# Kernel tuning notes

Measured on AMD Instinct MI355X. Metric: run time of the kernel, lower is better.

The kernel has to match this reference:

```python
import jax, jax.numpy as jnp
import numpy as np
from jax import lax

ANCHOR_AREAS = (128.0**2, 256.0**2, 512.0**2)
ASPECT_RATIOS = (0.5, 1.0, 2.0)
STRIDE = 32.0                      # resnet backbone: get_orig_stat maps fm -> input via x*32
PRE_NMS_TOP_N = 2000
POST_NMS_TOP_N = 100
NMS_IOU_T = 0.7
SCORE_T = 0.1
MIN_SCALE = 0.01
BBOX_XFORM_CLIP = float(np.log(1000.0 / 16.0))


def make_anchors(H, W):
    # anchors laid out in (H, W, A) order to match the offset permutation below
    sizes = []
    for area in ANCHOR_AREAS:
        for r in ASPECT_RATIOS:          # aspect_ratio = w / h
            sizes.append((np.sqrt(area * r), np.sqrt(area / r)))
    sizes = jnp.asarray(np.asarray(sizes, dtype=np.float32))  # [A, 2] (w, h)
    cy = (jnp.arange(H, dtype=jnp.float32) + 0.5) * STRIDE
    cx = (jnp.arange(W, dtype=jnp.float32) + 0.5) * STRIDE
    cyg, cxg = jnp.meshgrid(cy, cx, indexing='ij')             # [H, W]
    cxg = cxg[:, :, None]
    cyg = cyg[:, :, None]
    w = sizes[:, 0]
    h = sizes[:, 1]
    anchors = jnp.stack([cxg - w / 2, cyg - h / 2, cxg + w / 2, cyg + h / 2], axis=-1)
    return anchors.reshape(-1, 4)                              # [H*W*A, 4] xyxy


def decode_boxes(anchors, offsets):
    # anchors [N,4], offsets [B,N,4] (tx, ty, tw, th) -> boxes [B,N,4] xyxy
    wa = anchors[:, 2] - anchors[:, 0]
    ha = anchors[:, 3] - anchors[:, 1]
    cxa = anchors[:, 0] + 0.5 * wa
    cya = anchors[:, 1] + 0.5 * ha
    tx, ty = offsets[..., 0], offsets[..., 1]
    tw = jnp.minimum(offsets[..., 2], BBOX_XFORM_CLIP)
    th = jnp.minimum(offsets[..., 3], BBOX_XFORM_CLIP)
    px = tx * wa + cxa
    py = ty * ha + cya
    pw = jnp.exp(tw) * wa
    ph = jnp.exp(th) * ha
    return jnp.stack([px - pw / 2, py - ph / 2, px + pw / 2, py + ph / 2], axis=-1)


def box_iou(a, b):
    area_a = (a[:, 2] - a[:, 0]) * (a[:, 3] - a[:, 1])
    area_b = (b[:, 2] - b[:, 0]) * (b[:, 3] - b[:, 1])
    lt = jnp.maximum(a[:, None, :2], b[None, :, :2])
    rb = jnp.minimum(a[:, None, 2:], b[None, :, 2:])
    wh = jnp.clip(rb - lt, 0.0)
    inter = wh[..., 0] * wh[..., 1]
    return inter / (area_a[:, None] + area_b[None, :] - inter + 1e-9)


def nms_single(boxes, scores):
    # boxes [P,4] sorted by descending score; invalid entries carry score -1
    P = boxes.shape[0]
    iou = box_iou(boxes, boxes)
    idx = jnp.arange(P)

    def body(i, keep):
        sup = (iou[i] > NMS_IOU_T) & (idx > i)
        return jnp.where(keep[i], keep & (~sup), keep)

    keep = lax.stop_gradient(lax.fori_loop(0, P, body, scores > 0.0))
    kept_scores = jnp.where(keep, scores, -1.0)
    top_s, top_i = lax.top_k(kept_scores, POST_NMS_TOP_N)
    return boxes[top_i], top_s


def rpn_forward(features, W1, b1, W2, b2, W3, b3):
    B, Cin, H, W = features.shape
    A = W3.shape[0]
    # 3x3 sliding conv + ReLU
    t = lax.conv_general_dilated(
        features, W1, window_strides=(1, 1), padding='SAME',
        dimension_numbers=('NCHW', 'OIHW', 'NCHW'))
    t = jax.nn.relu(t + b1[None, :, None, None])
    # 1x1 sibling heads as channel contractions
    offs = jnp.einsum('bchw,oc->bohw', t, W2) + b2[None, :, None, None]   # [B, A*4, H, W]
    logits = jnp.einsum('bchw,oc->bohw', t, W3) + b3[None, :, None, None]  # [B, A, H, W]
    # reorder to per-anchor layout (H, W, A)
    offs = offs.reshape(B, A, 4, H, W).transpose(0, 3, 4, 1, 2).reshape(B, -1, 4)
    scores = jax.nn.sigmoid(logits.transpose(0, 2, 3, 1).reshape(B, -1))  # [B, N]
    anchors = make_anchors(H, W)
    boxes = decode_boxes(anchors, offs)                                    # [B, N, 4]
    # clip to image boundary (handle_cross_boundary_boxes during testing)
    img_w, img_h = W * STRIDE, H * STRIDE
    boxes = jnp.stack([
        jnp.clip(boxes[..., 0], 0.0, img_w),
        jnp.clip(boxes[..., 1], 0.0, img_h),
        jnp.clip(boxes[..., 2], 0.0, img_w),
        jnp.clip(boxes[..., 3], 0.0, img_h)], axis=-1)
    # score-threshold + min-scale filtering
    bw = boxes[..., 2] - boxes[..., 0]
    bh = boxes[..., 3] - boxes[..., 1]
    valid = (scores >= SCORE_T) & (bw > MIN_SCALE * img_w) & (bh > MIN_SCALE * img_h)
    masked = jnp.where(valid, scores, -1.0)
    # pre-NMS top-k, then per-image NMS + post-NMS top-n
    top_s, top_i = lax.top_k(masked, PRE_NMS_TOP_N)                        # [B, P]
    top_boxes = jnp.take_along_axis(boxes, top_i[..., None], axis=1)       # [B, P, 4]
    out_boxes, out_scores = jax.vmap(nms_single)(top_boxes, top_s)
    return out_boxes, out_scores                                           # [B,100,4], [B,100]


def setup_inputs() -> dict:
    key = jax.random.key(0)
    ks = jax.random.split(key, 4)
    B, Cin, H, W = 8, 1024, 50, 50
    A = 9
    C = 512
    return {
        'features': jax.random.normal(ks[0], (B, Cin, H, W), jnp.float32),
        'W1': jax.random.normal(ks[1], (C, Cin, 3, 3), jnp.float32) * 0.01,
        'b1': jnp.zeros((C,), jnp.float32),
        'W2': jax.random.normal(ks[2], (A * 4, C), jnp.float32) * 0.01,
        'b2': jnp.zeros((A * 4,), jnp.float32),
        'W3': jax.random.normal(ks[3], (A, C), jnp.float32) * 0.01,
        'b3': jnp.zeros((A,), jnp.float32),
    }


def reference(features, W1, b1, W2, b2, W3, b3):
    return rpn_forward(features, W1, b1, W2, b2, W3, b3)
```

## Files before the change

kernel.cpp:

```cpp
#include <hip/hip_runtime.h>
#include <cstdint>

#define NB 8
#define CIN 1024
#define HDIM 50
#define WDIM 50
#define COUT 512
#define NA 9
#define NANCH (HDIM*WDIM*NA)
#define PRE_N 2000
#define POST_N 100

typedef __attribute__((ext_vector_type(8))) short bf16x8;
typedef __attribute__((ext_vector_type(4))) float f32x4;
typedef __attribute__((ext_vector_type(16))) float f32x16;
typedef __attribute__((ext_vector_type(8))) unsigned short ushort8v;

constexpr size_t TPLANE    = 20578304;
constexpr size_t OFF_TPH   = 0;
constexpr size_t OFF_TPL   = 20578304;
constexpr size_t OFF_BOXES = 41156608;
constexpr size_t OFF_KEYS  = 44036608;
constexpr size_t OFF_TBOX  = 45476608;
constexpr size_t OFF_TS    = 45732608;
constexpr size_t OFF_SUP   = 45796608;
constexpr size_t QDIM      = 2976;
constexpr size_t PLSTRIDE  = QDIM * 8;
constexpr size_t PPLANE    = 48758784;
constexpr size_t OFF_PH    = 49892864;
constexpr size_t OFF_PL    = OFF_PH + PPLANE;
constexpr size_t WPLANE    = 9437184;
constexpr size_t OFF_WH    = 147410432;
constexpr size_t OFF_WL    = OFF_WH + WPLANE;

__device__ __forceinline__ void split2bf16(float v, unsigned short &hi, unsigned short &lo) {
    unsigned int u = __float_as_uint(v);
    unsigned int r = u + 0x7FFFu + ((u >> 16) & 1u);
    hi = (unsigned short)(r >> 16);
    float hf = __uint_as_float(((unsigned int)hi) << 16);
    float lf = v - hf;
    unsigned int u2 = __float_as_uint(lf);
    unsigned int r2 = u2 + 0x7FFFu + ((u2 >> 16) & 1u);
    lo = (unsigned short)(r2 >> 16);
}

__device__ __forceinline__ void gl_lds(const unsigned short* g, unsigned short* l) {
    __builtin_amdgcn_global_load_lds(
        (const __attribute__((address_space(1))) unsigned int*)(const void*)g,
        (__attribute__((address_space(3))) unsigned int*)(void*)l,
        16, 0, 0);
}

__global__ __launch_bounds__(256) void prep_all(const float* __restrict__ f,
                                                const float* __restrict__ W1,
                                                unsigned short* __restrict__ Ph,
                                                unsigned short* __restrict__ Pl,
                                                unsigned short* __restrict__ Wh,
                                                unsigned short* __restrict__ Wl) {
    int blk = blockIdx.x;
    if (blk < 5952) {
        int id = blk * 256 + threadIdx.x;
        int q = id % (int)QDIM; int r = id / (int)QDIM;
        int cic = r % 64; int b = r / 64;
        int pp = q - 53;
        int rr = pp / 52, cc = pp - rr * 52;
        int h = rr - 1, w = cc - 1;
        bool inb = (pp >= 0) && (pp < 2704) && (h >= 0) && (h < HDIM) && (w >= 0) && (w < WDIM);
        ushort8v hv0, lv0, hv1, lv1;
#pragma unroll
        for (int j = 0; j < 16; ++j) {
            float v = 0.f;
            if (inb) v = f[(((size_t)b * CIN + cic * 16 + j) * HDIM + h) * WDIM + w];
            unsigned short hi, lo;
            split2bf16(v, hi, lo);
            if (j < 8) { hv0[j] = hi; lv0[j] = lo; }
            else       { hv1[j - 8] = hi; lv1[j - 8] = lo; }
        }
        size_t b0 = ((size_t)((b * 64 + cic) * 2 + 0)) * PLSTRIDE + (size_t)q * 8;
        size_t b1 = ((size_t)((b * 64 + cic) * 2 + 1)) * PLSTRIDE + (size_t)q * 8;
        *(ushort8v*)&Ph[b0] = hv0;
        *(ushort8v*)&Ph[b1] = hv1;
        *(ushort8v*)&Pl[b0] = lv0;
        *(ushort8v*)&Pl[b1] = lv1;
    } else {
        int id = (blk - 5952) * 256 + threadIdx.x;
        int co = id % 64; int r = id / 64;
        int cic = r % 64; int cot = r / 64;
        int cog = cot * 64 + co;
        const float* src = W1 + ((size_t)cog * CIN + cic * 16) * 9;
        float v[144];
#pragma unroll
        for (int i = 0; i < 36; ++i) {
            float4 x = ((const float4*)src)[i];
            v[i * 4 + 0] = x.x; v[i * 4 + 1] = x.y; v[i * 4 + 2] = x.z; v[i * 4 + 3] = x.w;
        }
#pragma unroll
        for (int tap = 0; tap < 9; ++tap) {
            ushort8v hv0, lv0, hv1, lv1;
#pragma unroll
            for (int j = 0; j < 16; ++j) {
                unsigned short hi, lo;
                split2bf16(v[j * 9 + tap], hi, lo);
                if (j < 8) { hv0[j] = hi; lv0[j] = lo; }
                else       { hv1[j - 8] = hi; lv1[j - 8] = lo; }
            }
            size_t base = (((size_t)(cot * 64 + cic) * 9 + tap) * 2) * 512;
            *(ushort8v*)&Wh[base + co * 8]       = hv0;
            *(ushort8v*)&Wh[base + 512 + co * 8] = hv1;
            *(ushort8v*)&Wl[base + co * 8]       = lv0;
            *(ushort8v*)&Wl[base + 512 + co * 8] = lv1;
        }
    }
}


#define MFMA12(A_, B_)                                                               \
    do {                                                                             \
        _Pragma("unroll") for (int s_ = 0; s_ < 3; ++s_)                             \
        _Pragma("unroll") for (int jm_ = 0; jm_ < 2; ++jm_)                          \
        _Pragma("unroll") for (int jn_ = 0; jn_ < 2; ++jn_) {                        \
            const bf16x8 &av_ = (s_ == 2) ? A_[jm_][1] : A_[jm_][0];                 \
            const bf16x8 &bv_ = (s_ == 1) ? B_[jn_][1] : B_[jn_][0];                 \
            acc[jm_][jn_] = __builtin_amdgcn_mfma_f32_32x32x16_bf16(                 \
                av_, bv_, acc[jm_][jn_], 0, 0, 0);                                   \
        }                                                                            \
    } while (0)

#define LOADF(A_, B_, TL_)                                                           \
    do {                                                                             \
        const int dlt_ = (tg - 1) * 52 + ((TL_) - 1);                                \
        _Pragma("unroll") for (int jm_ = 0; jm_ < 2; ++jm_) {                        \
            int ad_ = ((wv * 2 + jm_) * 32 + lm + dlt_ + 53) * 8;                    \
            A_[jm_][0] = *(const bf16x8*)&bA[(0 * 2 + lk) * 3072 + ad_];             \
            A_[jm_][1] = *(const bf16x8*)&bA[(1 * 2 + lk) * 3072 + ad_];             \
        }                                                                            \
        _Pragma("unroll") for (int jn_ = 0; jn_ < 2; ++jn_) {                        \
            int bd_ = (TL_) * 1024 + lk * 512 + (jn_ * 32 + lm) * 8;                 \
            B_[jn_][0] = *(const bf16x8*)&bB[bd_];                                   \
            B_[jn_][1] = *(const bf16x8*)&bB[3072 + bd_];                            \
        }                                                                            \
    } while (0)

__global__ __launch_bounds__(256, 2) void conv_mfma(const unsigned short* __restrict__ FPh,
                                                    const unsigned short* __restrict__ FPl,
                                                    const unsigned short* __restrict__ WPh,
                                                    const unsigned short* __restrict__ WPl,
                                                    const float* __restrict__ b1,
                                                    unsigned short* __restrict__ Tph,
                                                    unsigned short* __restrict__ Tpl) {
    extern __shared__ unsigned short smem[];
    unsigned short* const Abase = smem;
    unsigned short* const Bbase = smem + 24576;

    int blk = blockIdx.x;
    int logical = (blk & 7) * 88 + (blk >> 3);
    int cot = logical & 7;
    int ptile = (logical >> 3) % 11;
    int b = logical / 88;
    int co0 = cot * 64;
    int P0 = 32 + ptile * 256;

    int t = threadIdx.x, wv = t >> 6, ln = t & 63;
    int lm = ln & 31, lk = ln >> 5;

    f32x16 acc[2][2];
#pragma unroll
    for (int jm = 0; jm < 2; ++jm)
#pragma unroll
        for (int jn = 0; jn < 2; ++jn)
#pragma unroll
            for (int rg = 0; rg < 16; ++rg) acc[jm][jn][rg] = 0.f;

    auto stageA = [&](int buf, int cic, int ac) {
        int hl = ac / 12, lkc = (ac / 6) & 1, s = ac % 6;
        const unsigned short* pl = hl ? FPl : FPh;
        const unsigned short* src = pl
            + ((size_t)((b * 64 + cic) * 2 + lkc)) * PLSTRIDE
            + (size_t)P0 * 8 + s * 512 + ln * 8;
        gl_lds(src, &Abase[buf * 12288 + (hl * 2 + lkc) * 3072 + s * 512]);
    };
    auto stageB = [&](int buf, int cic, int tg, int c) {
        int hl = c / 6, j = c % 6;
        const unsigned short* pl = hl ? WPl : WPh;
        const unsigned short* src = pl + (size_t)(cot * 64 + cic) * 9216
            + (size_t)(tg * 6 + j) * 512 + ln * 8;
        gl_lds(src, &Bbase[buf * 6144 + hl * 3072 + j * 512]);
    };

#pragma unroll
    for (int k = 0; k < 9; ++k) {
        int id = wv * 9 + k;
        if (id < 24) stageA(0, 0, id);
        else         stageB(0, 0, 0, id - 24);
    }
    __syncthreads();

#pragma unroll 1
    for (int cic = 0; cic < 64; ++cic) {
        int abuf = cic & 1;
        bool haveA = (cic + 1 < 64);
#pragma unroll
        for (int tg = 0; tg < 3; ++tg) {
            int bbuf = (cic + tg) & 1;
            int cicb = (tg == 2) ? cic + 1 : cic;
            int tgn  = (tg == 2) ? 0 : tg + 1;
            bool haveB = (cicb < 64);
#pragma unroll
            for (int k = 0; k < 5; ++k) {
                int id = wv * 5 + k;
                if (id < 12) { if (haveB) stageB(bbuf ^ 1, cicb, tgn, id); }
                else         { if (haveA) stageA(abuf ^ 1, cic + 1, tg * 8 + (id - 12)); }
            }
            const unsigned short* bA = Abase + abuf * 12288;
            const unsigned short* bB = Bbase + bbuf * 6144;

            bf16x8 aX[2][2], bX[2][2], aY[2][2], bY[2][2];
            LOADF(aX, bX, 0);
            __builtin_amdgcn_s_setprio(1);
            LOADF(aY, bY, 1);
            MFMA12(aX, bX);
            LOADF(aX, bX, 2);
            MFMA12(aY, bY);
            MFMA12(aX, bX);
            __builtin_amdgcn_s_setprio(0);

            __builtin_amdgcn_sched_group_barrier(0x070, 5, 0);
            __builtin_amdgcn_sched_group_barrier(0x100, 8, 0);
#pragma unroll
            for (int g = 0; g < 8; ++g) {
                __builtin_amdgcn_sched_group_barrier(0x008, 3, 0);
                __builtin_amdgcn_sched_group_barrier(0x100, 2, 0);
            }
            __builtin_amdgcn_sched_group_barrier(0x008, 12, 0);

            __syncthreads();
        }
    }

#pragma unroll
    for (int jn = 0; jn < 2; ++jn) {
        int co = co0 + jn * 32 + lm;
        float bv = b1[co];
#pragma unroll
        for (int jm = 0; jm < 2; ++jm) {
#pragma unroll
            for (int rg = 0; rg < 16; ++rg) {
                int mrow = (rg & 3) + 8 * (rg >> 2) + 4 * lk;
                int pp = P0 + (wv * 2 + jm) * 32 + mrow;
                int rr = pp / 52, cc = pp - rr * 52;
                int h = rr - 1, w = cc - 1;
                if ((unsigned)h < HDIM && (unsigned)w < WDIM) {
                    float v = fmaxf(acc[jm][jn][rg] + bv, 0.f);
                    unsigned short hi, lo;
                    split2bf16(v, hi, lo);
                    int px = b * 2500 + h * 50 + w;
                    size_t sa = (((((size_t)(px >> 7) * 16 + (co >> 5)) * 8 + ((px >> 4) & 7)) * 4
                                  + ((co >> 3) & 3)) * 16 + (px & 15)) * 8 + (co & 7);
                    Tph[sa] = hi;
                    Tpl[sa] = lo;
                }
            }
        }
    }
}

__global__ __launch_bounds__(256) void proj_decode_mfma(const unsigned short* __restrict__ Tph,
                                                        const unsigned short* __restrict__ Tpl,
                                                        const float* __restrict__ W2,
                                                        const float* __restrict__ b2,
                                                        const float* __restrict__ W3,
                                                        const float* __restrict__ b3,
                                                        float* __restrict__ boxes,
                                                        unsigned long long* __restrict__ keys) {
    __shared__ unsigned short sTh[4096], sTl[4096];
    __shared__ unsigned short sWh[1536], sWl[1536];
    __shared__ float pout[128 * 46];

    int blk = blockIdx.x;
    int px0 = blk * 128;
    int t = threadIdx.x, wv = t >> 6, ln = t & 63;
    int lm = ln & 15, q = ln >> 4;

    f32x4 acc[2][3];
#pragma unroll
    for (int jm = 0; jm < 2; ++jm)
#pragma unroll
        for (int nf = 0; nf < 3; ++nf) acc[jm][nf] = (f32x4){0.f, 0.f, 0.f, 0.f};

#pragma unroll 1
    for (int cc16 = 0; cc16 < 16; ++cc16) {
        __syncthreads();
        size_t base = ((size_t)blk * 16 + cc16) * 4096;
        if (wv == 0) {
#pragma unroll
            for (int s = 0; s < 4; ++s) gl_lds(Tph + base + s * 512 + ln * 8, &sTh[s * 512]);
        } else if (wv == 1) {
#pragma unroll
            for (int s = 4; s < 8; ++s) gl_lds(Tph + base + s * 512 + ln * 8, &sTh[s * 512]);
        } else if (wv == 2) {
#pragma unroll
            for (int s = 0; s < 4; ++s) gl_lds(Tpl + base + s * 512 + ln * 8, &sTl[s * 512]);
        } else {
#pragma unroll
            for (int s = 4; s < 8; ++s) gl_lds(Tpl + base + s * 512 + ln * 8, &sTl[s * 512]);
        }
        int c0 = cc16 * 32;
        for (int idx = t; idx < 1536; idx += 256) {
            int o = idx >> 5, ci = idx & 31;
            float v = 0.f;
            if (o < 36) v = W2[o * 512 + c0 + ci];
            else if (o < 45) v = W3[(o - 36) * 512 + c0 + ci];
            unsigned short hi, lo;
            split2bf16(v, hi, lo);
            int ad = (((o >> 4) * 4 + (ci >> 3)) * 16 + (o & 15)) * 8 + (ci & 7);
            sWh[ad] = hi; sWl[ad] = lo;
        }
        __syncthreads();

        bf16x8 a[2][2], bb[3][2];
#pragma unroll
        for (int jm = 0; jm < 2; ++jm) {
            int mf = wv * 2 + jm;
            int ad = ((mf * 4 + q) * 16 + lm) * 8;
            a[jm][0] = *(const bf16x8*)&sTh[ad];
            a[jm][1] = *(const bf16x8*)&sTl[ad];
        }
#pragma unroll
        for (int nf = 0; nf < 3; ++nf) {
            int ad = ((nf * 4 + q) * 16 + lm) * 8;
            bb[nf][0] = *(const bf16x8*)&sWh[ad];
            bb[nf][1] = *(const bf16x8*)&sWl[ad];
        }
#pragma unroll
        for (int jm = 0; jm < 2; ++jm)
#pragma unroll
            for (int nf = 0; nf < 3; ++nf) {
                acc[jm][nf] = __builtin_amdgcn_mfma_f32_16x16x32_bf16(a[jm][0], bb[nf][0], acc[jm][nf], 0, 0, 0);
                acc[jm][nf] = __builtin_amdgcn_mfma_f32_16x16x32_bf16(a[jm][0], bb[nf][1], acc[jm][nf], 0, 0, 0);
                acc[jm][nf] = __builtin_amdgcn_mfma_f32_16x16x32_bf16(a[jm][1], bb[nf][0], acc[jm][nf], 0, 0, 0);
            }
    }
    __syncthreads();
#pragma unroll
    for (int jm = 0; jm < 2; ++jm)
#pragma unroll
        for (int nf = 0; nf < 3; ++nf) {
            int o = nf * 16 + lm;
            if (o < 45) {
                float bias = (o < 36) ? b2[o] : b3[o - 36];
#pragma unroll
                for (int rg = 0; rg < 4; ++rg) {
                    int pxl = (wv * 2 + jm) * 16 + q * 4 + rg;
                    pout[pxl * 46 + o] = acc[jm][nf][rg] + bias;
                }
            }
        }
    __syncthreads();

    const float AW[9] = {90.50966799187809f, 128.0f, 181.01933598375618f,
                         181.01933598375618f, 256.0f, 362.03867196751236f,
                         362.03867196751236f, 512.0f, 724.0773439350247f};
    const float AH[9] = {181.01933598375618f, 128.0f, 90.50966799187809f,
                         362.03867196751236f, 256.0f, 181.01933598375618f,
                         724.0773439350247f, 512.0f, 362.03867196751236f};
    const float CLIPV = 4.135166556742356f;
    const float IMG = 1600.0f;

    for (int it = t; it < 128 * 9; it += 256) {
        int pxl = it / 9, a = it - pxl * 9;
        int pxg = px0 + pxl;
        if (pxg >= 20000) continue;
        int b = pxg / 2500, rem = pxg % 2500;
        int h = rem / 50, w = rem % 50;

        float tx = pout[pxl * 46 + a * 4 + 0];
        float ty = pout[pxl * 46 + a * 4 + 1];
        float tw = pout[pxl * 46 + a * 4 + 2];
        float th = pout[pxl * 46 + a * 4 + 3];
        float lg = pout[pxl * 46 + 36 + a];

        float s = 1.0f / (1.0f + expf(-lg));

        float cx = ((float)w + 0.5f) * 32.0f;
        float cy = ((float)h + 0.5f) * 32.0f;
        float x1a = cx - 0.5f * AW[a];
        float x2a = cx + 0.5f * AW[a];
        float y1a = cy - 0.5f * AH[a];
        float y2a = cy + 0.5f * AH[a];
        float waf = x2a - x1a;
        float haf = y2a - y1a;
        float cxa = x1a + 0.5f * waf;
        float cya = y1a + 0.5f * haf;

        float twc = tw < CLIPV ? tw : CLIPV;
        float thc = th < CLIPV ? th : CLIPV;
        float pxc = tx * waf + cxa;
        float pyc = ty * haf + cya;
        float pw  = expf(twc) * waf;
        float ph  = expf(thc) * haf;

        float x1 = pxc - 0.5f * pw;
        float y1 = pyc - 0.5f * ph;
        float x2 = pxc + 0.5f * pw;
        float y2 = pyc + 0.5f * ph;
        x1 = fminf(fmaxf(x1, 0.f), IMG);
        y1 = fminf(fmaxf(y1, 0.f), IMG);
        x2 = fminf(fmaxf(x2, 0.f), IMG);
        y2 = fminf(fmaxf(y2, 0.f), IMG);

        float bw = x2 - x1, bh = y2 - y1;
        bool valid = (s >= 0.1f) && (bw > 16.0f) && (bh > 16.0f);
        float m = valid ? s : -1.0f;

        int idx = (h * WDIM + w) * NA + a;
        size_t gi = (size_t)b * NANCH + idx;
        ((float4*)boxes)[gi] = make_float4(x1, y1, x2, y2);
        unsigned int u = __float_as_uint(m);
        unsigned int k32 = (u & 0x80000000u) ? ~u : (u | 0x80000000u);
        keys[gi] = ((unsigned long long)k32 << 15) | (unsigned long long)(32767 - idx);
    }
}

__global__ __launch_bounds__(1024) void select_sort_kernel(const unsigned long long* __restrict__ keys,
                                                           const float* __restrict__ boxes,
                                                           float* __restrict__ top_boxes,
                                                           float* __restrict__ top_s) {
    int b = blockIdx.x;
    int t = threadIdx.x;
    int wv = t >> 6;
    const unsigned long long* kb = keys + (size_t)b * NANCH;

    __shared__ unsigned int whist[16][256];
    __shared__ unsigned int hist[256];
    __shared__ int s_chosen, s_rnew;
    __shared__ unsigned int s_cnt;
    __shared__ unsigned long long skeys[2048];

    const int widths[6] = {8, 8, 8, 8, 8, 7};
    unsigned long long prefix = 0;
    int bitsdone = 0;
    int r = PRE_N;

    for (int p = 0; p < 6; ++p) {
        int width = widths[p];
        int bins = 1 << width;
        int shift = 47 - bitsdone - width;
        for (int i = t; i < 16 * 256; i += 1024) ((unsigned int*)whist)[i] = 0;
        __syncthreads();
        for (int i = t; i < NANCH; i += 1024) {
            unsigned long long k = kb[i];
            if ((k >> (47 - bitsdone)) == prefix)
                atomicAdd(&whist[wv][(unsigned)((k >> shift) & (unsigned long long)(bins - 1))], 1u);
        }
        __syncthreads();
        if (t < bins) {
            unsigned int s = 0;
#pragma unroll
            for (int w = 0; w < 16; ++w) s += whist[w][t];
            hist[t] = s;
        }
        __syncthreads();
        if (t == 0) {
            int acc = 0, chosen = 0, rnew = 1;
            for (int d = bins - 1; d >= 0; --d) {
                int hv = (int)hist[d];
                if (acc + hv >= r) { chosen = d; rnew = r - acc; break; }
                acc += hv;
            }
            s_chosen = chosen;
            s_rnew = rnew;
        }
        __syncthreads();
        prefix = (prefix << width) | (unsigned long long)s_chosen;
        bitsdone += width;
        r = s_rnew;
        __syncthreads();
    }
    unsigned long long Kst = prefix;

    if (t == 0) s_cnt = 0;
    __syncthreads();
    for (int i = t; i < NANCH; i += 1024) {
        unsigned long long k = kb[i];
        if (k >= Kst) {
            unsigned int p = atomicAdd(&s_cnt, 1u);
            if (p < 2048) skeys[p] = k;
        }
    }
    __syncthreads();
    unsigned int cnt = s_cnt;
    for (int i = t; i < 2048; i += 1024)
        if (i >= (int)cnt) skeys[i] = 0ull;
    for (int k = 2; k <= 2048; k <<= 1) {
        for (int j = k >> 1; j > 0; j >>= 1) {
            __syncthreads();
            for (int i = t; i < 2048; i += 1024) {
                int l = i ^ j;
                if (l > i) {
                    unsigned long long a = skeys[i], c = skeys[l];
                    bool up = ((i & k) == 0);
                    if (up ? (a < c) : (a > c)) { skeys[i] = c; skeys[l] = a; }
                }
            }
        }
    }
    __syncthreads();
    for (int i = t; i < PRE_N; i += 1024) {
        unsigned long long k = skeys[i];
        unsigned int k32 = (unsigned int)(k >> 15);
        float m = (k32 & 0x80000000u) ? __uint_as_float(k32 & 0x7FFFFFFFu)
                                      : __uint_as_float(~k32);
        unsigned int idx = 32767u - (unsigned int)(k & 32767ull);
        size_t gi = (size_t)b * NANCH + idx;
        top_s[b * PRE_N + i] = m;
        ((float4*)top_boxes)[b * PRE_N + i] = ((const float4*)boxes)[gi];
    }
}

__global__ __launch_bounds__(256) void sup_kernel(const float* __restrict__ top_boxes,
                                                  unsigned long long* __restrict__ supm) {
    int blk = blockIdx.x;
    int b = blk / 125;
    int chunk = blk % 125;
    int t = threadIdx.x;

    __shared__ float bx1[PRE_N], by1[PRE_N], bx2[PRE_N], by2[PRE_N];
    for (int i = t; i < PRE_N; i += 256) {
        float4 v = ((const float4*)top_boxes)[b * PRE_N + i];
        bx1[i] = v.x; by1[i] = v.y; bx2[i] = v.z; by2[i] = v.w;
    }
    __syncthreads();

    int wave = t >> 6, lane = t & 63;
    for (int rr = 0; rr < 4; ++rr) {
        int i = chunk * 16 + wave * 4 + rr;
        float ax1 = bx1[i], ay1 = by1[i], ax2 = bx2[i], ay2 = by2[i];
        float aarea = (ax2 - ax1) * (ay2 - ay1);
        for (int jw = 0; jw < 32; ++jw) {
            int j = jw * 64 + lane;
            bool sup = false;
            if (j > i && j < PRE_N) {
                float jx1 = bx1[j], jy1 = by1[j], jx2 = bx2[j], jy2 = by2[j];
                float ix1 = fmaxf(ax1, jx1), iy1 = fmaxf(ay1, jy1);
                float ix2 = fminf(ax2, jx2), iy2 = fminf(ay2, jy2);
                float iw = fmaxf(ix2 - ix1, 0.f);
                float ih = fmaxf(iy2 - iy1, 0.f);
                float inter = iw * ih;
                float barea = (jx2 - jx1) * (jy2 - jy1);
                float iou = inter / (aarea + barea - inter + 1e-9f);
                sup = iou > 0.7f;
            }
            unsigned long long m = __ballot(sup);
            if (lane == 0) supm[((size_t)b * PRE_N + i) * 32 + jw] = m;
        }
    }
}

__global__ __launch_bounds__(256) void nms_fin_kernel(const float* __restrict__ top_s,
                                                      const unsigned long long* __restrict__ supm,
                                                      const float* __restrict__ top_boxes,
                                                      float* __restrict__ out) {
    int b = blockIdx.x;
    int t = threadIdx.x;
    __shared__ unsigned int kw[64];
    __shared__ int wpre[65];

    if (t < 64) {
        int lane = t;
        unsigned int alive = 0;
        for (int q = 0; q < 32; ++q) {
            int i = lane * 32 + q;
            if (i < PRE_N && top_s[b * PRE_N + i] > 0.f) alive |= (1u << q);
        }
        const unsigned long long* sm = supm + (size_t)b * PRE_N * 32;
        const unsigned int* sup32 = (const unsigned int*)sm;

        for (int tt = 0; tt < 32; ++tt) {
            unsigned int alo = __shfl(alive, 2 * tt);
            unsigned int ahi = __shfl(alive, 2 * tt + 1);
            unsigned long long talive = (unsigned long long)alo | ((unsigned long long)ahi << 32);
            int i_row = tt * 64 + lane;
            unsigned long long rm = (i_row < PRE_N) ? sm[(size_t)i_row * 32 + tt] : 0ull;

            unsigned long long kept = 0, rem = talive;
            while (rem) {
                int j = __builtin_ctzll(rem);
                kept |= (1ull << j);
                unsigned long long rmj = __shfl(rm, j);
                rem &= ~rmj;
                rem &= ~(1ull << j);
            }

            unsigned int oracc = 0;
            unsigned long long kk = kept;
            while (kk) {
                int j0 = __builtin_ctzll(kk); kk &= kk - 1;
                int j1 = -1, j2 = -1, j3 = -1;
                if (kk) { j1 = __builtin_ctzll(kk); kk &= kk - 1; }
                if (kk) { j2 = __builtin_ctzll(kk); kk &= kk - 1; }
                if (kk) { j3 = __builtin_ctzll(kk); kk &= kk - 1; }
                unsigned int v0 = sup32[(size_t)(tt * 64 + j0) * 64 + lane];
                unsigned int v1 = (j1 >= 0) ? sup32[(size_t)(tt * 64 + j1) * 64 + lane] : 0u;
                unsigned int v2 = (j2 >= 0) ? sup32[(size_t)(tt * 64 + j2) * 64 + lane] : 0u;
                unsigned int v3 = (j3 >= 0) ? sup32[(size_t)(tt * 64 + j3) * 64 + lane] : 0u;
                oracc |= v0 | v1 | v2 | v3;
            }
            alive &= ~oracc;
            if (lane == 2 * tt)     alive = (unsigned int)kept;
            if (lane == 2 * tt + 1) alive = (unsigned int)(kept >> 32);
        }
        kw[lane] = alive;
    }
    __syncthreads();
    if (t == 0) {
        int run = 0;
        for (int w = 0; w < 64; ++w) { wpre[w] = run; run += __popc(kw[w]); }
        wpre[64] = run;
    }
    __syncthreads();
    int total = wpre[64];
    float* out_boxes  = out;
    float* out_scores = out + NB * POST_N * 4;
    for (int i = t; i < PRE_N; i += 256) {
        unsigned int w = kw[i >> 5];
        bool kept = (w >> (i & 31)) & 1u;
        int rk = wpre[i >> 5] + __popc(w & ((1u << (i & 31)) - 1u));
        int pos = kept ? rk : total + (i - rk);
        if (pos < POST_N) {
            out_scores[b * POST_N + pos] = kept ? top_s[b * PRE_N + i] : -1.0f;
            ((float4*)out_boxes)[b * POST_N + pos] = ((const float4*)top_boxes)[b * PRE_N + i];
        }
    }
}

extern "C" void kernel_launch(void* const* d_in, const int* in_sizes, int n_in,
                              void* d_out, int out_size, void* d_ws, size_t ws_size,
                              hipStream_t stream) {
    const float* features = (const float*)d_in[0];
    const float* W1 = (const float*)d_in[1];
    const float* b1 = (const float*)d_in[2];
    const float* W2 = (const float*)d_in[3];
    const float* b2 = (const float*)d_in[4];
    const float* W3 = (const float*)d_in[5];
    const float* b3 = (const float*)d_in[6];
    float* out = (float*)d_out;
    char* ws = (char*)d_ws;

    unsigned short* Tph = (unsigned short*)(ws + OFF_TPH);
    unsigned short* Tpl = (unsigned short*)(ws + OFF_TPL);
    float* boxes   = (float*)(ws + OFF_BOXES);
    unsigned long long* keys = (unsigned long long*)(ws + OFF_KEYS);
    float* top_boxes = (float*)(ws + OFF_TBOX);
    float* top_s     = (float*)(ws + OFF_TS);
    unsigned long long* supm = (unsigned long long*)(ws + OFF_SUP);
    unsigned short* FPh = (unsigned short*)(ws + OFF_PH);
    unsigned short* FPl = (unsigned short*)(ws + OFF_PL);
    unsigned short* WPh = (unsigned short*)(ws + OFF_WH);
    unsigned short* WPl = (unsigned short*)(ws + OFF_WL);

    static bool conv_attr_set = false;
    if (!conv_attr_set) {
        hipFuncSetAttribute(reinterpret_cast<const void*>(&conv_mfma),
                            hipFuncAttributeMaxDynamicSharedMemorySize, 73728);
        conv_attr_set = true;
    }

    prep_all<<<6080, 256, 0, stream>>>(features, W1, FPh, FPl, WPh, WPl);
    conv_mfma<<<704, 256, 73728, stream>>>(FPh, FPl, WPh, WPl, b1, Tph, Tpl);
    proj_decode_mfma<<<157, 256, 0, stream>>>(Tph, Tpl, W2, b2, W3, b3, boxes, keys);
    select_sort_kernel<<<NB, 1024, 0, stream>>>(keys, boxes, top_boxes, top_s);
    sup_kernel<<<NB * 125, 256, 0, stream>>>(top_boxes, supm);
    nms_fin_kernel<<<NB, 256, 0, stream>>>(top_s, supm, top_boxes, out);
}
```

Before: 1.083 ms.

## Rebalance conv staging, peel last K-step, early-exit radix select, widen NMS OR batch

The conv GEMM loop now gives every wave a fixed 3 B-tile and 2 A-tile stage (replacing the 5-per-wave split with idle slots) and peels the last input-channel chunk so it skips staging and scheduling barriers. The radix top-k select stops early once the candidate count at the current prefix fits in the 2048-entry sort buffer, saving histogram passes over all anchors. The NMS suppression OR loop batches 8 row loads instead of 4 for more memory-level parallelism. Early exit can admit more candidates into the bitonic sort, and the new staging split must still cover all tiles exactly.

New measurement: 1.001 ms. 1.08x faster.

```diff
diff --git a/kernel.cpp b/kernel.cpp
--- a/kernel.cpp
+++ b/kernel.cpp
@@ -51,6 +51,9 @@
         16, 0, 0);
 }
 
+struct StageOn  { static constexpr bool value = true;  };
+struct StageOff { static constexpr bool value = false; };
+
 __global__ __launch_bounds__(256) void prep_all(const float* __restrict__ f,
                                                 const float* __restrict__ W1,
                                                 unsigned short* __restrict__ Ph,
@@ -195,21 +198,21 @@
     }
     __syncthreads();
 
-#pragma unroll 1
-    for (int cic = 0; cic < 64; ++cic) {
+    auto do_cic = [&](int cic, auto stage_c) {
+        constexpr bool STAGE = decltype(stage_c)::value;
         int abuf = cic & 1;
-        bool haveA = (cic + 1 < 64);
 #pragma unroll
         for (int tg = 0; tg < 3; ++tg) {
             int bbuf = (cic + tg) & 1;
-            int cicb = (tg == 2) ? cic + 1 : cic;
-            int tgn  = (tg == 2) ? 0 : tg + 1;
-            bool haveB = (cicb < 64);
-#pragma unroll
-            for (int k = 0; k < 5; ++k) {
-                int id = wv * 5 + k;
-                if (id < 12) { if (haveB) stageB(bbuf ^ 1, cicb, tgn, id); }
-                else         { if (haveA) stageA(abuf ^ 1, cic + 1, tg * 8 + (id - 12)); }
+            if (STAGE || tg < 2) {
+                int cicb = (tg == 2) ? cic + 1 : cic;
+                int tgn  = (tg == 2) ? 0 : tg + 1;
+#pragma unroll
+                for (int j = 0; j < 3; ++j) stageB(bbuf ^ 1, cicb, tgn, wv * 3 + j);
+            }
+            if constexpr (STAGE) {
+#pragma unroll
+                for (int j = 0; j < 2; ++j) stageA(abuf ^ 1, cic + 1, tg * 8 + wv * 2 + j);
             }
             const unsigned short* bA = Abase + abuf * 12288;
             const unsigned short* bB = Bbase + bbuf * 6144;
@@ -224,18 +227,23 @@
             MFMA12(aX, bX);
             __builtin_amdgcn_s_setprio(0);
 
-            __builtin_amdgcn_sched_group_barrier(0x070, 5, 0);
-            __builtin_amdgcn_sched_group_barrier(0x100, 8, 0);
-#pragma unroll
-            for (int g = 0; g < 8; ++g) {
-                __builtin_amdgcn_sched_group_barrier(0x008, 3, 0);
-                __builtin_amdgcn_sched_group_barrier(0x100, 2, 0);
-            }
-            __builtin_amdgcn_sched_group_barrier(0x008, 12, 0);
-
+            if constexpr (STAGE) {
+                __builtin_amdgcn_sched_group_barrier(0x070, 5, 0);
+                __builtin_amdgcn_sched_group_barrier(0x100, 8, 0);
+#pragma unroll
+                for (int g = 0; g < 8; ++g) {
+                    __builtin_amdgcn_sched_group_barrier(0x008, 3, 0);
+                    __builtin_amdgcn_sched_group_barrier(0x100, 2, 0);
+                }
+                __builtin_amdgcn_sched_group_barrier(0x008, 12, 0);
+            }
             __syncthreads();
         }
-    }
+    };
+
+#pragma unroll 1
+    for (int cic = 0; cic < 63; ++cic) do_cic(cic, StageOn{});
+    do_cic(63, StageOff{});
 
 #pragma unroll
     for (int jn = 0; jn < 2; ++jn) {
@@ -432,7 +440,7 @@
 
     __shared__ unsigned int whist[16][256];
     __shared__ unsigned int hist[256];
-    __shared__ int s_chosen, s_rnew;
+    __shared__ int s_chosen, s_rnew, s_done;
     __shared__ unsigned int s_cnt;
     __shared__ unsigned long long skeys[2048];
 
@@ -440,6 +448,8 @@
     unsigned long long prefix = 0;
     int bitsdone = 0;
     int r = PRE_N;
+
+    if (t == 0) s_done = 0;
 
     for (int p = 0; p < 6; ++p) {
         int width = widths[p];
@@ -464,7 +474,11 @@
             int acc = 0, chosen = 0, rnew = 1;
             for (int d = bins - 1; d >= 0; --d) {
                 int hv = (int)hist[d];
-                if (acc + hv >= r) { chosen = d; rnew = r - acc; break; }
+                if (acc + hv >= r) {
+                    chosen = d; rnew = r - acc;
+                    if ((PRE_N - r) + acc + hv <= 2048) s_done = 1;
+                    break;
+                }
                 acc += hv;
             }
             s_chosen = chosen;
@@ -475,8 +489,9 @@
         bitsdone += width;
         r = s_rnew;
         __syncthreads();
-    }
-    unsigned long long Kst = prefix;
+        if (s_done) break;
+    }
+    unsigned long long Kst = prefix << (47 - bitsdone);
 
     if (t == 0) s_cnt = 0;
     __syncthreads();
@@ -595,15 +610,23 @@
             unsigned long long kk = kept;
             while (kk) {
                 int j0 = __builtin_ctzll(kk); kk &= kk - 1;
-                int j1 = -1, j2 = -1, j3 = -1;
+                int j1 = -1, j2 = -1, j3 = -1, j4 = -1, j5 = -1, j6 = -1, j7 = -1;
                 if (kk) { j1 = __builtin_ctzll(kk); kk &= kk - 1; }
                 if (kk) { j2 = __builtin_ctzll(kk); kk &= kk - 1; }
                 if (kk) { j3 = __builtin_ctzll(kk); kk &= kk - 1; }
+                if (kk) { j4 = __builtin_ctzll(kk); kk &= kk - 1; }
+                if (kk) { j5 = __builtin_ctzll(kk); kk &= kk - 1; }
+                if (kk) { j6 = __builtin_ctzll(kk); kk &= kk - 1; }
+                if (kk) { j7 = __builtin_ctzll(kk); kk &= kk - 1; }
                 unsigned int v0 = sup32[(size_t)(tt * 64 + j0) * 64 + lane];
                 unsigned int v1 = (j1 >= 0) ? sup32[(size_t)(tt * 64 + j1) * 64 + lane] : 0u;
                 unsigned int v2 = (j2 >= 0) ? sup32[(size_t)(tt * 64 + j2) * 64 + lane] : 0u;
                 unsigned int v3 = (j3 >= 0) ? sup32[(size_t)(tt * 64 + j3) * 64 + lane] : 0u;
-                oracc |= v0 | v1 | v2 | v3;
+                unsigned int v4 = (j4 >= 0) ? sup32[(size_t)(tt * 64 + j4) * 64 + lane] : 0u;
+                unsigned int v5 = (j5 >= 0) ? sup32[(size_t)(tt * 64 + j5) * 64 + lane] : 0u;
+                unsigned int v6 = (j6 >= 0) ? sup32[(size_t)(tt * 64 + j6) * 64 + lane] : 0u;
+                unsigned int v7 = (j7 >= 0) ? sup32[(size_t)(tt * 64 + j7) * 64 + lane] : 0u;
+                oracc |= (v0 | v1) | (v2 | v3) | (v4 | v5) | (v6 | v7);
             }
             alive &= ~oracc;
             if (lane == 2 * tt)     alive = (unsigned int)kept;
```
